# Kernel tuning notes

Measured on AMD Instinct MI355X. Metric: run time of the kernel, lower is better.

Reference implementation:

```python
import jax, jax.numpy as jnp
import numpy as np

B, DIM, H, W, HEADS = 8, 384, 128, 128, 8
C = DIM // HEADS  # per-head channels = 48
EPS_LN = 1e-5


def _conv1x1(x, w, b):
    # x: (b, cin, h, w), w: (cout, cin)
    return jnp.einsum('bchw,oc->bohw', x, w) + b[None, :, None, None]


def _dwconv3(x, w, b):
    # depthwise 3x3, w: (C, 1, 3, 3)
    y = jax.lax.conv_general_dilated(
        x, w, window_strides=(1, 1), padding='SAME',
        dimension_numbers=('NCHW', 'OIHW', 'NCHW'),
        feature_group_count=x.shape[1])
    return y + b[None, :, None, None]


def _layernorm2d(x, w, b):
    # normalize over channel dim per spatial location
    mu = jnp.mean(x, axis=1, keepdims=True)
    var = jnp.var(x, axis=1, keepdims=True)
    xn = (x - mu) * jax.lax.rsqrt(var + EPS_LN)
    return xn * w[None, :, None, None] + b[None, :, None, None]


def _l2norm(x):
    # F.normalize(x, dim=-1)
    n = jnp.sqrt(jnp.sum(x * x, axis=-1, keepdims=True))
    return x / jnp.maximum(n, 1e-12)


def setup_inputs() -> dict:
    key = jax.random.key(0)
    ks = jax.random.split(key, 16)
    w = lambda k, sh: jax.random.normal(k, sh, jnp.float32) * 0.02
    z = lambda sh: jnp.zeros(sh, jnp.float32)
    return {
        'T_E_input': jax.random.normal(ks[0], (B, DIM, H, W), jnp.float32),
        'C_E_input': jax.random.normal(ks[1], (B, DIM, H, W), jnp.float32),
        'tn_w': jnp.ones((DIM,), jnp.float32), 'tn_b': z((DIM,)),
        'cn_w': jnp.ones((DIM,), jnp.float32), 'cn_b': z((DIM,)),
        'tq_w': w(ks[2], (DIM, DIM)), 'tq_b': z((DIM,)),
        'tq_dw': w(ks[3], (DIM, 1, 3, 3)), 'tq_db': z((DIM,)),
        'ck_w': w(ks[4], (DIM, DIM)), 'ck_b': z((DIM,)),
        'ck_dw': w(ks[5], (DIM, 1, 3, 3)), 'ck_db': z((DIM,)),
        'cv_w': w(ks[6], (DIM, DIM)), 'cv_b': z((DIM,)),
        'cv_dw': w(ks[7], (DIM, 1, 3, 3)), 'cv_db': z((DIM,)),
        'temperature': jnp.ones((1, 1, 1), jnp.float32),
        'proj_w': w(ks[8], (DIM, DIM)), 'proj_b': z((DIM,)),
        'a1': jnp.array([0.2], jnp.float32), 'a2': jnp.array([0.2], jnp.float32),
        'a3': jnp.array([0.2], jnp.float32), 'a4': jnp.array([0.2], jnp.float32),
    }


def reference(T_E_input, C_E_input, tn_w, tn_b, cn_w, cn_b,
              tq_w, tq_b, tq_dw, tq_db, ck_w, ck_b, ck_dw, ck_db,
              cv_w, cv_b, cv_dw, cv_db, temperature, proj_w, proj_b,
              a1, a2, a3, a4):
    b, c, h, w = T_E_input.shape
    T_E = _layernorm2d(T_E_input, tn_w, tn_b)
    C_E = _layernorm2d(C_E_input, cn_w, cn_b)

    q = _dwconv3(_conv1x1(T_E, tq_w, tq_b), tq_dw, tq_db)
    k = _dwconv3(_conv1x1(C_E, ck_w, ck_b), ck_dw, ck_db)
    v = _dwconv3(_conv1x1(C_E, cv_w, cv_b), cv_dw, cv_db)

    hw = h * w
    q = _l2norm(q.reshape(b, HEADS, C, hw))  # (b, head, C, hw)
    k = _l2norm(k.reshape(b, HEADS, C, hw))
    v = v.reshape(b, HEADS, C, hw)

    # (b, head, C, C) channel attention
    attn = jnp.einsum('bhcn,bhdn->bhcd', q, k) * temperature

    k1, k2, k3, k4 = C // 2, C * 2 // 3, C * 3 // 4, C * 4 // 5  # 24,32,36,38
    # one top-k gives all four thresholds (values sorted descending)
    vals = jax.lax.top_k(attn, k4)[0]

    def masked_softmax_out(kk):
        thresh = vals[..., kk - 1:kk]
        a = jnp.where(attn >= thresh, attn, -jnp.inf)
        a = jax.nn.softmax(a, axis=-1)
        return jnp.einsum('bhcd,bhdn->bhcn', a, v)

    out = (masked_softmax_out(k1) * a1 + masked_softmax_out(k2) * a2 +
           masked_softmax_out(k3) * a3 + masked_softmax_out(k4) * a4)

    fusion = out.reshape(b, c, h, w)
    fusion = _conv1x1(fusion, proj_w, proj_b) + C_E_input
    return fusion
```

## Files before the change

kernel.cpp:

```cpp
#include <hip/hip_runtime.h>
#include <hip/hip_bf16.h>
#include <math.h>

#define HW   16384
#define WD   128
#define DIM  384
#define NB   8
#define NH   8
#define NC   48
#define NPIX (NB*HW)
#define MAT  (DIM*DIM)

typedef __hip_bfloat16 bf16;
typedef short s16x8 __attribute__((ext_vector_type(8)));
typedef float f32x4 __attribute__((ext_vector_type(4)));

__device__ __forceinline__ float b2f(bf16 x){ return __bfloat162float(x); }
__device__ __forceinline__ bf16  f2b(float x){ return __float2bfloat16(x); }
__device__ __forceinline__ unsigned short f2bu(float x){
  bf16 b = __float2bfloat16(x);
  unsigned short u;
  __builtin_memcpy(&u, &b, 2);
  return u;
}
__device__ __forceinline__ float u2f(unsigned short u){
  union{ unsigned int i; float f; } x;
  x.i = ((unsigned int)u) << 16;
  return x.f;
}

__global__ void k_zero(float* p, int n){
  int i = blockIdx.x*256 + threadIdx.x;
  if(i < n) p[i] = 0.f;
}

__global__ __launch_bounds__(256) void k_stats(const float* __restrict__ T,
                                               const float* __restrict__ C,
                                               float* __restrict__ mu,
                                               float* __restrict__ rstd){
  int t = threadIdx.x;
  int P = blockIdx.x*256 + t;
  const float* src = (blockIdx.y == 0) ? T : C;
  int b = P >> 14, p = P & (HW-1);
  const float* base = src + (size_t)b*DIM*HW + p;
  float s = 0.f, ss = 0.f;
  for(int c = 0; c < DIM; c++){
    float v = base[(size_t)c*HW];
    s += v; ss += v*v;
  }
  float m   = s * (1.f/DIM);
  float var = ss * (1.f/DIM) - m*m;
  float rs  = rsqrtf(var + 1e-5f);
  int o = blockIdx.y*NPIX + P;
  mu[o] = m; rstd[o] = rs;
}

__global__ void k_prep(const float* tq_w, const float* ck_w, const float* cv_w,
                       const float* tq_b, const float* ck_b, const float* cv_b,
                       const float* tn_w, const float* tn_b,
                       const float* cn_w, const float* cn_b,
                       bf16* Wpb, float* c1, float* c2){
  int o = blockIdx.x, conv = blockIdx.y, t = threadIdx.x;
  const float* W  = conv==0 ? tq_w : (conv==1 ? ck_w : cv_w);
  const float* cb = conv==0 ? tq_b : (conv==1 ? ck_b : cv_b);
  const float* lw = conv==0 ? tn_w : cn_w;
  const float* lb = conv==0 ? tn_b : cn_b;
  float s1 = 0.f, s2 = 0.f;
  for(int c = t; c < DIM; c += 64){
    float w  = W[o*DIM + c];
    float wp = w * lw[c];
    bf16 wb  = f2b(wp);
    Wpb[conv*MAT + o*DIM + c] = wb;
    s1 += w * lb[c];
    s2 += b2f(wb);
  }
  for(int off = 32; off; off >>= 1){ s1 += __shfl_down(s1, off); s2 += __shfl_down(s2, off); }
  if(t == 0){ c1[conv*DIM + o] = s1 + cb[o]; c2[conv*DIM + o] = s2; }
}

template<int MODE>
__global__ __launch_bounds__(256) void k_gmm(
    const float* __restrict__ Bf, const bf16* __restrict__ Bh,
    const unsigned short* __restrict__ A,
    const float* __restrict__ bias, const float* __restrict__ c2,
    const float* __restrict__ mu, const float* __restrict__ rstd,
    const float* __restrict__ resid,
    bf16* __restrict__ dsth, float* __restrict__ dstf){
  __shared__ unsigned short As[4096];
  __shared__ unsigned short Bs[4096];
  const int t = threadIdx.x;
  const int l = t & 63;
  const int w = t >> 6;
  const int wr = w >> 1, wc = w & 1;
  const int b = blockIdx.z;
  const int o0 = blockIdx.y*128, p0 = blockIdx.x*128;
  const unsigned short* Aw = A + (MODE==1 ? (size_t)b*MAT : (size_t)0);

  f32x4 zero = {0.f, 0.f, 0.f, 0.f};
  f32x4 acc[4][4];
  #pragma unroll
  for(int m = 0; m < 4; m++)
    #pragma unroll
    for(int n = 0; n < 4; n++) acc[m][n] = zero;

  const int a_kb = t & 3, a_o = t >> 2;
  const int b_cl = t >> 4;
  const int b_p8 = (t & 15)*8;
  const int kbr = l >> 4;
  const int lr  = l & 15;

  for(int c0 = 0; c0 < DIM; c0 += 32){
    #pragma unroll
    for(int r = 0; r < 2; r++){
      int oo = a_o + 64*r;
      s16x8 av = *(const s16x8*)(Aw + (size_t)(o0 + oo)*DIM + c0 + a_kb*8);
      int ad = (a_kb*2048 + oo*16) ^ (a_kb<<5);
      *(s16x8*)((char*)As + ad) = av;
    }
    #pragma unroll
    for(int r = 0; r < 2; r++){
      int cl = b_cl + 16*r;
      int c  = c0 + cl;
      unsigned short vals[8];
      if(MODE == 0){
        const float* src = Bf + ((size_t)(b*DIM + c))*HW + p0 + b_p8;
        float4 x0 = *(const float4*)src;
        float4 x1 = *(const float4*)(src + 4);
        vals[0]=f2bu(x0.x); vals[1]=f2bu(x0.y); vals[2]=f2bu(x0.z); vals[3]=f2bu(x0.w);
        vals[4]=f2bu(x1.x); vals[5]=f2bu(x1.y); vals[6]=f2bu(x1.z); vals[7]=f2bu(x1.w);
      } else {
        const unsigned short* src = (const unsigned short*)Bh + ((size_t)(b*DIM + c))*HW + p0 + b_p8;
        s16x8 v = *(const s16x8*)src;
        #pragma unroll
        for(int j = 0; j < 8; j++) vals[j] = (unsigned short)v[j];
      }
      int base = (cl>>3)*2048 + (cl&7)*2;
      #pragma unroll
      for(int j8 = 0; j8 < 8; j8++){
        int pp = b_p8 + j8;
        int ad = (base + pp*16) ^ (((pp>>3)&7)<<4);
        *(unsigned short*)((char*)Bs + ad) = vals[j8];
      }
    }
    __syncthreads();
    s16x8 af[4], bv[4];
    #pragma unroll
    for(int m = 0; m < 4; m++){
      int oo = wr*64 + m*16 + lr;
      int ad = (kbr*2048 + oo*16) ^ (kbr<<5);
      af[m] = *(const s16x8*)((const char*)As + ad);
    }
    #pragma unroll
    for(int n = 0; n < 4; n++){
      int pp = wc*64 + n*16 + lr;
      int ad = (kbr*2048 + pp*16) ^ (((pp>>3)&7)<<4);
      bv[n] = *(const s16x8*)((const char*)Bs + ad);
    }
    #pragma unroll
    for(int m = 0; m < 4; m++)
      #pragma unroll
      for(int n = 0; n < 4; n++)
        acc[m][n] = __builtin_amdgcn_mfma_f32_16x16x32_bf16(af[m], bv[n], acc[m][n], 0, 0, 0);
    __syncthreads();
  }

  #pragma unroll
  for(int m = 0; m < 4; m++){
    int ob = o0 + wr*64 + m*16 + (l>>4)*4;
    #pragma unroll
    for(int n = 0; n < 4; n++){
      int p = p0 + wc*64 + n*16 + (l&15);
      #pragma unroll
      for(int r4 = 0; r4 < 4; r4++){
        int o = ob + r4;
        size_t oidx = ((size_t)(b*DIM + o))*HW + p;
        float v = acc[m][n][r4];
        if(MODE == 0){
          int P = b*HW + p;
          float rs = rstd[P], mm = mu[P];
          dsth[oidx] = f2b(rs*v + bias[o] - mm*rs*c2[o]);
        } else {
          dstf[oidx] = v + bias[o] + resid[oidx];
        }
      }
    }
  }
}

__global__ __launch_bounds__(256) void k_dw(const bf16* __restrict__ src, bf16* __restrict__ dst,
                                            const float* __restrict__ dw, const float* __restrict__ db,
                                            float* __restrict__ nrm){
  __shared__ unsigned short tile[34*136];
  __shared__ float red[4];
  int t = threadIdx.x;
  int tb = blockIdx.x;
  int c = blockIdx.y, b = blockIdx.z;
  size_t base = (size_t)(b*DIM + c)*HW;
  int y0 = tb*32;
  const unsigned short* sp = (const unsigned short*)src + base;
  for(int i = t; i < 544; i += 256){
    int r = i >> 4, ch = i & 15;
    int yy = y0 + r - 1;
    s16x8 v = {};
    if(yy >= 0 && yy < 128) v = *(const s16x8*)(sp + yy*WD + ch*8);
    *(s16x8*)&tile[r*136 + ch*8] = v;
  }
  float w[9];
  #pragma unroll
  for(int i = 0; i < 9; i++) w[i] = dw[c*9 + i];
  float bias = db[c];
  __syncthreads();
  unsigned short* dp = (unsigned short*)dst + base;
  float ssq = 0.f;
  #pragma unroll
  for(int task = 0; task < 2; task++){
    int i = t + task*256;
    int ry = i >> 4, xseg = i & 15;
    int xb = xseg*8;
    float v[3][10];
    #pragma unroll
    for(int rr = 0; rr < 3; rr++){
      const unsigned short* row = &tile[(ry+rr)*136];
      s16x8 mid = *(const s16x8*)&row[xb];
      v[rr][0] = (xb == 0)   ? 0.f : u2f(row[xb-1]);
      #pragma unroll
      for(int j = 0; j < 8; j++) v[rr][1+j] = u2f((unsigned short)mid[j]);
      v[rr][9] = (xb == 120) ? 0.f : u2f(row[xb+8]);
    }
    s16x8 outv;
    #pragma unroll
    for(int j = 0; j < 8; j++){
      float s = bias;
      #pragma unroll
      for(int rr = 0; rr < 3; rr++){
        s = fmaf(w[rr*3+0], v[rr][j],   s);
        s = fmaf(w[rr*3+1], v[rr][j+1], s);
        s = fmaf(w[rr*3+2], v[rr][j+2], s);
      }
      ssq = fmaf(s, s, ssq);
      outv[j] = (short)f2bu(s);
    }
    *(s16x8*)(dp + (y0+ry)*WD + xb) = outv;
  }
  if(nrm){
    for(int off = 32; off; off >>= 1) ssq += __shfl_down(ssq, off);
    if((t & 63) == 0) red[t >> 6] = ssq;
    __syncthreads();
    if(t == 0) atomicAdd(&nrm[b*DIM + c], red[0]+red[1]+red[2]+red[3]);
  }
}

__global__ __launch_bounds__(256) void k_attn(const bf16* __restrict__ q, const bf16* __restrict__ k,
                                              float* __restrict__ attn){
  __shared__ float part[4][48][49];
  const int t = threadIdx.x;
  const int l = t & 63;
  const int w = t >> 6;
  const int split = blockIdx.x;
  const int h = blockIdx.y, b = blockIdx.z;
  const unsigned short* qb = (const unsigned short*)q + (size_t)(b*DIM + h*NC)*HW;
  const unsigned short* kb = (const unsigned short*)k + (size_t)(b*DIM + h*NC)*HW;
  const int row = l & 15;
  const int kch = (l >> 4)*8;

  f32x4 zero = {0.f, 0.f, 0.f, 0.f};
  f32x4 acc[3][3];
  #pragma unroll
  for(int m = 0; m < 3; m++)
    #pragma unroll
    for(int n = 0; n < 3; n++) acc[m][n] = zero;

  const int n0 = split*2048 + w*512;
  for(int nn = 0; nn < 512; nn += 32){
    s16x8 qa[3], ka[3];
    #pragma unroll
    for(int m = 0; m < 3; m++)
      qa[m] = *(const s16x8*)(qb + (size_t)(m*16 + row)*HW + n0 + nn + kch);
    #pragma unroll
    for(int n = 0; n < 3; n++)
      ka[n] = *(const s16x8*)(kb + (size_t)(n*16 + row)*HW + n0 + nn + kch);
    #pragma unroll
    for(int m = 0; m < 3; m++)
      #pragma unroll
      for(int n = 0; n < 3; n++)
        acc[m][n] = __builtin_amdgcn_mfma_f32_16x16x32_bf16(qa[m], ka[n], acc[m][n], 0, 0, 0);
  }

  #pragma unroll
  for(int m = 0; m < 3; m++)
    #pragma unroll
    for(int n = 0; n < 3; n++)
      #pragma unroll
      for(int r = 0; r < 4; r++)
        part[w][m*16 + (l>>4)*4 + r][n*16 + (l&15)] = acc[m][n][r];
  __syncthreads();

  float* ab = attn + (size_t)(b*NH + h)*NC*NC;
  #pragma unroll
  for(int i = t; i < NC*NC; i += 256){
    int rr = i / NC, cc = i % NC;
    float s = part[0][rr][cc] + part[1][rr][cc] + part[2][rr][cc] + part[3][rr][cc];
    atomicAdd(&ab[i], s);
  }
}

__global__ void k_pmat(const float* __restrict__ attn, const float* __restrict__ nq,
                       const float* __restrict__ nk, const float* __restrict__ tptr,
                       const float* __restrict__ a1p, const float* __restrict__ a2p,
                       const float* __restrict__ a3p, const float* __restrict__ a4p,
                       float* __restrict__ P){
  int t = threadIdx.x;
  int h = blockIdx.x, b = blockIdx.y;
  __shared__ float nkv[48];
  if(t < 48) nkv[t] = fmaxf(sqrtf(nk[b*DIM + h*NC + t]), 1e-12f);
  __syncthreads();
  if(t >= 48) return;
  int c = t;
  float temp = tptr[0];
  float nqc = fmaxf(sqrtf(nq[b*DIM + h*NC + c]), 1e-12f);
  const float* row = attn + ((size_t)(b*NH + h)*NC + c)*NC;
  float r[48], s[48];
  for(int d = 0; d < 48; d++){
    float v = row[d] * temp / (nqc * nkv[d]);
    r[d] = v; s[d] = v;
  }
  for(int i = 1; i < 48; i++){
    float key = s[i]; int j = i-1;
    while(j >= 0 && s[j] < key){ s[j+1] = s[j]; j--; }
    s[j+1] = key;
  }
  float m  = s[0];
  float t1 = s[23], t2 = s[31], t3 = s[35], t4 = s[37];
  float d1 = 0.f, d2 = 0.f, d3 = 0.f, d4 = 0.f;
  for(int d = 0; d < 48; d++){
    float e = expf(r[d] - m);
    s[d] = e;
    if(r[d] >= t1) d1 += e;
    if(r[d] >= t2) d2 += e;
    if(r[d] >= t3) d3 += e;
    if(r[d] >= t4) d4 += e;
  }
  float w1 = a1p[0]/d1, w2 = a2p[0]/d2, w3 = a3p[0]/d3, w4 = a4p[0]/d4;
  float* Pr = P + ((size_t)(b*NH + h)*NC + c)*NC;
  for(int d = 0; d < 48; d++){
    float wsum = 0.f;
    if(r[d] >= t1) wsum += w1;
    if(r[d] >= t2) wsum += w2;
    if(r[d] >= t3) wsum += w3;
    if(r[d] >= t4) wsum += w4;
    Pr[d] = s[d] * wsum;
  }
}

__global__ __launch_bounds__(384) void k_w2(const float* __restrict__ Wp, const float* __restrict__ P,
                                            bf16* __restrict__ W2){
  int t = threadIdx.x;
  int o = blockIdx.x, b = blockIdx.y;
  int h = t / 48, d = t % 48;
  const float* Pb = P + (size_t)(b*NH + h)*NC*NC + d;
  const float* Wr = Wp + o*DIM + h*NC;
  float s = 0.f;
  for(int c = 0; c < 48; c++) s = fmaf(Wr[c], Pb[c*NC], s);
  W2[((size_t)b*DIM + o)*DIM + t] = f2b(s);
}

extern "C" void kernel_launch(void* const* d_in, const int* in_sizes, int n_in,
                              void* d_out, int out_size, void* d_ws, size_t ws_size,
                              hipStream_t stream){
  const float* TEin = (const float*)d_in[0];
  const float* CEin = (const float*)d_in[1];
  const float* tn_w = (const float*)d_in[2];
  const float* tn_b = (const float*)d_in[3];
  const float* cn_w = (const float*)d_in[4];
  const float* cn_b = (const float*)d_in[5];
  const float* tq_w = (const float*)d_in[6];
  const float* tq_b = (const float*)d_in[7];
  const float* tq_dw= (const float*)d_in[8];
  const float* tq_db= (const float*)d_in[9];
  const float* ck_w = (const float*)d_in[10];
  const float* ck_b = (const float*)d_in[11];
  const float* ck_dw= (const float*)d_in[12];
  const float* ck_db= (const float*)d_in[13];
  const float* cv_w = (const float*)d_in[14];
  const float* cv_b = (const float*)d_in[15];
  const float* cv_dw= (const float*)d_in[16];
  const float* cv_db= (const float*)d_in[17];
  const float* temp = (const float*)d_in[18];
  const float* pj_w = (const float*)d_in[19];
  const float* pj_b = (const float*)d_in[20];
  const float* a1   = (const float*)d_in[21];
  const float* a2   = (const float*)d_in[22];
  const float* a3   = (const float*)d_in[23];
  const float* a4   = (const float*)d_in[24];

  char* ws = (char*)d_ws;
  const size_t S2 = (size_t)NB*DIM*HW*2;
  bf16* q0 = (bf16*)(ws);
  bf16* k0 = (bf16*)(ws +   S2);
  bf16* v0 = (bf16*)(ws + 2*S2);
  bf16* q1 = (bf16*)(ws + 3*S2);
  bf16* k1 = (bf16*)(ws);
  bf16* v1 = (bf16*)(ws +   S2);
  char* sm = ws + 4*S2;
  float* mu   = (float*)(sm);
  float* rstd = (float*)(sm + 1048576);
  bf16*  Wpb  = (bf16*) (sm + 2097152);
  float* c1   = (float*)(sm + 3866624);
  float* c2   = (float*)(sm + 3871232);
  float* nq   = (float*)(sm + 3875840);
  float* nk   = (float*)(sm + 3888128);
  float* attn = (float*)(sm + 3900416);
  float* P    = (float*)(sm + 4490240);
  bf16*  W2b  = (bf16*) (sm + 5080064);

  k_zero<<<dim3(600), 256, 0, stream>>>(nq, 153600);
  k_stats<<<dim3(512, 2), 256, 0, stream>>>(TEin, CEin, mu, rstd);
  k_prep<<<dim3(384, 3), 64, 0, stream>>>(tq_w, ck_w, cv_w, tq_b, ck_b, cv_b,
                                          tn_w, tn_b, cn_w, cn_b, Wpb, c1, c2);
  k_gmm<0><<<dim3(128,3,8), 256, 0, stream>>>(TEin, nullptr, (const unsigned short*)Wpb,
                                              c1, c2, mu, rstd, nullptr, q0, nullptr);
  k_gmm<0><<<dim3(128,3,8), 256, 0, stream>>>(CEin, nullptr, (const unsigned short*)(Wpb+MAT),
                                              c1+DIM, c2+DIM, mu+NPIX, rstd+NPIX, nullptr, k0, nullptr);
  k_gmm<0><<<dim3(128,3,8), 256, 0, stream>>>(CEin, nullptr, (const unsigned short*)(Wpb+2*MAT),
                                              c1+2*DIM, c2+2*DIM, mu+NPIX, rstd+NPIX, nullptr, v0, nullptr);
  k_dw<<<dim3(4,384,8), 256, 0, stream>>>(q0, q1, tq_dw, tq_db, nq);
  k_dw<<<dim3(4,384,8), 256, 0, stream>>>(k0, k1, ck_dw, ck_db, nk);
  k_dw<<<dim3(4,384,8), 256, 0, stream>>>(v0, v1, cv_dw, cv_db, nullptr);
  k_attn<<<dim3(8,8,8), 256, 0, stream>>>(q1, k1, attn);
  k_pmat<<<dim3(8,8), 64, 0, stream>>>(attn, nq, nk, temp, a1, a2, a3, a4, P);
  k_w2<<<dim3(384,8), 384, 0, stream>>>(pj_w, P, W2b);
  k_gmm<1><<<dim3(128,3,8), 256, 0, stream>>>(nullptr, v1, (const unsigned short*)W2b,
                                              pj_b, nullptr, nullptr, nullptr, CEin, nullptr, (float*)d_out);
}
```

Baseline: 1.298 ms.

## Materialize normalized bf16 activations in layernorm pass and read bf16 in GEMMs

The stats kernel now also writes the layer-normalized inputs as bf16 tensors, staging each pixel column in shared memory. The three input GEMMs then read half-width bf16 instead of fp32, and C_E is converted only once instead of twice. The mu/rstd/c2 correction in the epilogue is removed. B-tile staging now packs two channels per 32-bit LDS store. Buffers are reassigned to hold the extra normalized tensors. The cost is an extra write and read of two bf16 activation tensors, plus rounding after normalization rather than before.

```diff
diff --git a/kernel.cpp b/kernel.cpp
--- a/kernel.cpp
+++ b/kernel.cpp
@@ -34,57 +34,68 @@
   if(i < n) p[i] = 0.f;
 }
 
-__global__ __launch_bounds__(256) void k_stats(const float* __restrict__ T,
-                                               const float* __restrict__ C,
-                                               float* __restrict__ mu,
-                                               float* __restrict__ rstd){
+__global__ __launch_bounds__(256) void k_ln(const float* __restrict__ T,
+                                            const float* __restrict__ C,
+                                            bf16* __restrict__ Tn,
+                                            bf16* __restrict__ Cn){
+  __shared__ unsigned short xs[DIM*64];
+  __shared__ float sred[4][64], ssred[4][64];
+  __shared__ float mv[64], rv[64];
   int t = threadIdx.x;
-  int P = blockIdx.x*256 + t;
+  int px = t & 63, part = t >> 6;
+  int P = blockIdx.x*64 + px;
   const float* src = (blockIdx.y == 0) ? T : C;
+  bf16* dst = (blockIdx.y == 0) ? Tn : Cn;
   int b = P >> 14, p = P & (HW-1);
   const float* base = src + (size_t)b*DIM*HW + p;
   float s = 0.f, ss = 0.f;
-  for(int c = 0; c < DIM; c++){
+  for(int c = part*96; c < part*96 + 96; c++){
     float v = base[(size_t)c*HW];
     s += v; ss += v*v;
-  }
-  float m   = s * (1.f/DIM);
-  float var = ss * (1.f/DIM) - m*m;
-  float rs  = rsqrtf(var + 1e-5f);
-  int o = blockIdx.y*NPIX + P;
-  mu[o] = m; rstd[o] = rs;
+    xs[c*64 + px] = f2bu(v);
+  }
+  sred[part][px] = s; ssred[part][px] = ss;
+  __syncthreads();
+  if(t < 64){
+    float S  = sred[0][t]+sred[1][t]+sred[2][t]+sred[3][t];
+    float SS = ssred[0][t]+ssred[1][t]+ssred[2][t]+ssred[3][t];
+    float m  = S * (1.f/DIM);
+    float var = SS * (1.f/DIM) - m*m;
+    mv[t] = m; rv[t] = rsqrtf(var + 1e-5f);
+  }
+  __syncthreads();
+  float m = mv[px], rs = rv[px];
+  bf16* ob = dst + (size_t)b*DIM*HW + p;
+  for(int c = part*96; c < part*96 + 96; c++){
+    float v = u2f(xs[c*64 + px]);
+    ob[(size_t)c*HW] = f2b((v - m)*rs);
+  }
 }
 
 __global__ void k_prep(const float* tq_w, const float* ck_w, const float* cv_w,
                        const float* tq_b, const float* ck_b, const float* cv_b,
                        const float* tn_w, const float* tn_b,
                        const float* cn_w, const float* cn_b,
-                       bf16* Wpb, float* c1, float* c2){
+                       bf16* Wpb, float* c1){
   int o = blockIdx.x, conv = blockIdx.y, t = threadIdx.x;
   const float* W  = conv==0 ? tq_w : (conv==1 ? ck_w : cv_w);
   const float* cb = conv==0 ? tq_b : (conv==1 ? ck_b : cv_b);
   const float* lw = conv==0 ? tn_w : cn_w;
   const float* lb = conv==0 ? tn_b : cn_b;
-  float s1 = 0.f, s2 = 0.f;
+  float s1 = 0.f;
   for(int c = t; c < DIM; c += 64){
     float w  = W[o*DIM + c];
-    float wp = w * lw[c];
-    bf16 wb  = f2b(wp);
-    Wpb[conv*MAT + o*DIM + c] = wb;
+    Wpb[conv*MAT + o*DIM + c] = f2b(w * lw[c]);
     s1 += w * lb[c];
-    s2 += b2f(wb);
-  }
-  for(int off = 32; off; off >>= 1){ s1 += __shfl_down(s1, off); s2 += __shfl_down(s2, off); }
-  if(t == 0){ c1[conv*DIM + o] = s1 + cb[o]; c2[conv*DIM + o] = s2; }
+  }
+  for(int off = 32; off; off >>= 1) s1 += __shfl_down(s1, off);
+  if(t == 0) c1[conv*DIM + o] = s1 + cb[o];
 }
 
 template<int MODE>
 __global__ __launch_bounds__(256) void k_gmm(
-    const float* __restrict__ Bf, const bf16* __restrict__ Bh,
-    const unsigned short* __restrict__ A,
-    const float* __restrict__ bias, const float* __restrict__ c2,
-    const float* __restrict__ mu, const float* __restrict__ rstd,
-    const float* __restrict__ resid,
+    const bf16* __restrict__ Bh, const unsigned short* __restrict__ A,
+    const float* __restrict__ bias, const float* __restrict__ resid,
     bf16* __restrict__ dsth, float* __restrict__ dstf){
   __shared__ unsigned short As[4096];
   __shared__ unsigned short Bs[4096];
@@ -104,7 +115,7 @@
     for(int n = 0; n < 4; n++) acc[m][n] = zero;
 
   const int a_kb = t & 3, a_o = t >> 2;
-  const int b_cl = t >> 4;
+  const int b_cp = (t >> 4)*2;
   const int b_p8 = (t & 15)*8;
   const int kbr = l >> 4;
   const int lr  = l & 15;
@@ -117,29 +128,20 @@
       int ad = (a_kb*2048 + oo*16) ^ (a_kb<<5);
       *(s16x8*)((char*)As + ad) = av;
     }
-    #pragma unroll
-    for(int r = 0; r < 2; r++){
-      int cl = b_cl + 16*r;
-      int c  = c0 + cl;
-      unsigned short vals[8];
-      if(MODE == 0){
-        const float* src = Bf + ((size_t)(b*DIM + c))*HW + p0 + b_p8;
-        float4 x0 = *(const float4*)src;
-        float4 x1 = *(const float4*)(src + 4);
-        vals[0]=f2bu(x0.x); vals[1]=f2bu(x0.y); vals[2]=f2bu(x0.z); vals[3]=f2bu(x0.w);
-        vals[4]=f2bu(x1.x); vals[5]=f2bu(x1.y); vals[6]=f2bu(x1.z); vals[7]=f2bu(x1.w);
-      } else {
-        const unsigned short* src = (const unsigned short*)Bh + ((size_t)(b*DIM + c))*HW + p0 + b_p8;
-        s16x8 v = *(const s16x8*)src;
-        #pragma unroll
-        for(int j = 0; j < 8; j++) vals[j] = (unsigned short)v[j];
-      }
-      int base = (cl>>3)*2048 + (cl&7)*2;
+    {
+      const unsigned short* src = (const unsigned short*)Bh
+          + ((size_t)(b*DIM + c0 + b_cp))*HW + p0 + b_p8;
+      s16x8 v0 = *(const s16x8*)src;
+      s16x8 v1 = *(const s16x8*)(src + HW);
+      int kb = b_cp >> 3, j = b_cp & 7;
+      int basead = kb*2048 + j*2;
       #pragma unroll
       for(int j8 = 0; j8 < 8; j8++){
         int pp = b_p8 + j8;
-        int ad = (base + pp*16) ^ (((pp>>3)&7)<<4);
-        *(unsigned short*)((char*)Bs + ad) = vals[j8];
+        int ad = (basead + pp*16) ^ (((pp>>3)&7)<<4);
+        unsigned int pk = (unsigned int)(unsigned short)v0[j8]
+                        | ((unsigned int)(unsigned short)v1[j8] << 16);
+        *(unsigned int*)((char*)Bs + ad) = pk;
       }
     }
     __syncthreads();
@@ -174,14 +176,9 @@
       for(int r4 = 0; r4 < 4; r4++){
         int o = ob + r4;
         size_t oidx = ((size_t)(b*DIM + o))*HW + p;
-        float v = acc[m][n][r4];
-        if(MODE == 0){
-          int P = b*HW + p;
-          float rs = rstd[P], mm = mu[P];
-          dsth[oidx] = f2b(rs*v + bias[o] - mm*rs*c2[o]);
-        } else {
-          dstf[oidx] = v + bias[o] + resid[oidx];
-        }
+        float v = acc[m][n][r4] + bias[o];
+        if(MODE == 0) dsth[oidx] = f2b(v);
+        else          dstf[oidx] = v + resid[oidx];
       }
     }
   }
@@ -395,18 +392,13 @@
 
   char* ws = (char*)d_ws;
   const size_t S2 = (size_t)NB*DIM*HW*2;
-  bf16* q0 = (bf16*)(ws);
-  bf16* k0 = (bf16*)(ws +   S2);
-  bf16* v0 = (bf16*)(ws + 2*S2);
-  bf16* q1 = (bf16*)(ws + 3*S2);
-  bf16* k1 = (bf16*)(ws);
-  bf16* v1 = (bf16*)(ws +   S2);
+  bf16* bufA = (bf16*)(ws);
+  bf16* bufB = (bf16*)(ws +   S2);
+  bf16* bufC = (bf16*)(ws + 2*S2);
+  bf16* bufD = (bf16*)(ws + 3*S2);
   char* sm = ws + 4*S2;
-  float* mu   = (float*)(sm);
-  float* rstd = (float*)(sm + 1048576);
   bf16*  Wpb  = (bf16*) (sm + 2097152);
   float* c1   = (float*)(sm + 3866624);
-  float* c2   = (float*)(sm + 3871232);
   float* nq   = (float*)(sm + 3875840);
   float* nk   = (float*)(sm + 3888128);
   float* attn = (float*)(sm + 3900416);
@@ -414,21 +406,21 @@
   bf16*  W2b  = (bf16*) (sm + 5080064);
 
   k_zero<<<dim3(600), 256, 0, stream>>>(nq, 153600);
-  k_stats<<<dim3(512, 2), 256, 0, stream>>>(TEin, CEin, mu, rstd);
+  k_ln<<<dim3(2048, 2), 256, 0, stream>>>(TEin, CEin, bufA, bufD);
   k_prep<<<dim3(384, 3), 64, 0, stream>>>(tq_w, ck_w, cv_w, tq_b, ck_b, cv_b,
-                                          tn_w, tn_b, cn_w, cn_b, Wpb, c1, c2);
-  k_gmm<0><<<dim3(128,3,8), 256, 0, stream>>>(TEin, nullptr, (const unsigned short*)Wpb,
-                                              c1, c2, mu, rstd, nullptr, q0, nullptr);
-  k_gmm<0><<<dim3(128,3,8), 256, 0, stream>>>(CEin, nullptr, (const unsigned short*)(Wpb+MAT),
-                                              c1+DIM, c2+DIM, mu+NPIX, rstd+NPIX, nullptr, k0, nullptr);
-  k_gmm<0><<<dim3(128,3,8), 256, 0, stream>>>(CEin, nullptr, (const unsigned short*)(Wpb+2*MAT),
-                                              c1+2*DIM, c2+2*DIM, mu+NPIX, rstd+NPIX, nullptr, v0, nullptr);
-  k_dw<<<dim3(4,384,8), 256, 0, stream>>>(q0, q1, tq_dw, tq_db, nq);
-  k_dw<<<dim3(4,384,8), 256, 0, stream>>>(k0, k1, ck_dw, ck_db, nk);
-  k_dw<<<dim3(4,384,8), 256, 0, stream>>>(v0, v1, cv_dw, cv_db, nullptr);
-  k_attn<<<dim3(8,8,8), 256, 0, stream>>>(q1, k1, attn);
+                                          tn_w, tn_b, cn_w, cn_b, Wpb, c1);
+  k_gmm<0><<<dim3(128,3,8), 256, 0, stream>>>(bufD, (const unsigned short*)(Wpb+MAT),
+                                              c1+DIM, nullptr, bufB, nullptr);
+  k_gmm<0><<<dim3(128,3,8), 256, 0, stream>>>(bufD, (const unsigned short*)(Wpb+2*MAT),
+                                              c1+2*DIM, nullptr, bufC, nullptr);
+  k_gmm<0><<<dim3(128,3,8), 256, 0, stream>>>(bufA, (const unsigned short*)Wpb,
+                                              c1, nullptr, bufD, nullptr);
+  k_dw<<<dim3(4,384,8), 256, 0, stream>>>(bufD, bufA, tq_dw, tq_db, nq);
+  k_dw<<<dim3(4,384,8), 256, 0, stream>>>(bufB, bufD, ck_dw, ck_db, nk);
+  k_dw<<<dim3(4,384,8), 256, 0, stream>>>(bufC, bufB, cv_dw, cv_db, nullptr);
+  k_attn<<<dim3(8,8,8), 256, 0, stream>>>(bufA, bufD, attn);
   k_pmat<<<dim3(8,8), 64, 0, stream>>>(attn, nq, nk, temp, a1, a2, a3, a4, P);
   k_w2<<<dim3(384,8), 384, 0, stream>>>(pj_w, P, W2b);
-  k_gmm<1><<<dim3(128,3,8), 256, 0, stream>>>(nullptr, v1, (const unsigned short*)W2b,
-                                              pj_b, nullptr, nullptr, nullptr, CEin, nullptr, (float*)d_out);
-}
+  k_gmm<1><<<dim3(128,3,8), 256, 0, stream>>>(bufB, (const unsigned short*)W2b,
+                                              pj_b, CEin, nullptr, (float*)d_out);
+}
```

Result: faster. 1.236 ms (-4.8%).
